# Kernel tuning notes

Measured on AMD Instinct MI355X. Metric: run time of the kernel, lower is better.

## Reference

```python
import jax, jax.numpy as jnp
import numpy as np

NHEAD = 16
EPS = 1e-5


def layer_norm(x, w, b):
    mu = jnp.mean(x, axis=-1, keepdims=True)
    var = jnp.var(x, axis=-1, keepdims=True)
    return (x - mu) * jax.lax.rsqrt(var + EPS) * w + b


def setup_inputs() -> dict:
    key = jax.random.key(0)
    ks = jax.random.split(key, 14)
    B, S, E, F = 16, 1024, 1024, 4096
    s = 0.02
    return {
        "x": jax.random.normal(ks[0], (B, S, E), jnp.float32),
        "in_proj_w": jax.random.normal(ks[1], (3 * E, E), jnp.float32) * s,
        "in_proj_b": jax.random.normal(ks[2], (3 * E,), jnp.float32) * s,
        "out_w": jax.random.normal(ks[3], (E, E), jnp.float32) * s,
        "out_b": jax.random.normal(ks[4], (E,), jnp.float32) * s,
        "lin1_w": jax.random.normal(ks[5], (F, E), jnp.float32) * s,
        "lin1_b": jax.random.normal(ks[6], (F,), jnp.float32) * s,
        "lin2_w": jax.random.normal(ks[7], (E, F), jnp.float32) * s,
        "lin2_b": jax.random.normal(ks[8], (E,), jnp.float32) * s,
        "norm1_w": jnp.ones((E,), jnp.float32),
        "norm1_b": jnp.zeros((E,), jnp.float32),
        "norm2_w": jnp.ones((E,), jnp.float32),
        "norm2_b": jnp.zeros((E,), jnp.float32),
    }


def reference(x, in_proj_w, in_proj_b, out_w, out_b, lin1_w, lin1_b, lin2_w, lin2_b,
              norm1_w, norm1_b, norm2_w, norm2_b):
    B, S, E = x.shape
    H = NHEAD
    D = E // H

    # --- pre-norm self-attention (q = k = v = norm1(x)) ---
    xn = layer_norm(x, norm1_w, norm1_b)
    qkv = xn @ in_proj_w.T + in_proj_b                      # [B,S,3E]
    q, k, v = jnp.split(qkv, 3, axis=-1)
    q = q.reshape(B, S, H, D)
    k = k.reshape(B, S, H, D)
    v = v.reshape(B, S, H, D)
    scale = 1.0 / jnp.sqrt(jnp.asarray(D, x.dtype))
    scores = jnp.einsum("bqhd,bkhd->bhqk", q, k) * scale    # [B,H,S,S]
    attn = jax.nn.softmax(scores, axis=-1)
    ctx = jnp.einsum("bhqk,bkhd->bqhd", attn, v).reshape(B, S, E)
    attn_out = ctx @ out_w.T + out_b
    x = x + attn_out

    # --- pre-norm feedforward (gelu) ---
    xn2 = layer_norm(x, norm2_w, norm2_b)
    h = jax.nn.gelu(xn2 @ lin1_w.T + lin1_b, approximate=False)
    x = x + (h @ lin2_w.T + lin2_b)
    return x
```

## Files before the change

### kernel.cpp

```cpp
#include <hip/hip_runtime.h>


typedef __attribute__((ext_vector_type(8))) short bf16x8;
typedef __attribute__((ext_vector_type(4))) float f32x4;
typedef __attribute__((ext_vector_type(8))) unsigned short u16x8;
typedef __attribute__((ext_vector_type(4))) unsigned short u16x4;

__device__ __forceinline__ float bf2f(unsigned short u) {
    return __uint_as_float(((unsigned int)u) << 16);
}
__device__ __forceinline__ unsigned short f2bf(float f) {
    unsigned int u = __float_as_uint(f);
    u += 0x7fffu + ((u >> 16) & 1u);
    return (unsigned short)(u >> 16);
}
__device__ __forceinline__ unsigned int pkbf_trunc(float a, float b) {
    return (__float_as_uint(a) >> 16) | (__float_as_uint(b) & 0xffff0000u);
}

__device__ __forceinline__ float fast_gelu(float v) {
    const float x = v * 0.70710678118654752f;
    const float ax = fabsf(x);
    const float t = __builtin_amdgcn_rcpf(fmaf(0.3275911f, ax, 1.0f));
    float p = fmaf(1.061405429f, t, -1.453152027f);
    p = fmaf(p, t, 1.421413741f);
    p = fmaf(p, t, -0.284496736f);
    p = fmaf(p, t, 0.254829592f);
    p = p * t;
    const float e = __expf(-x * x);
    float erfv = fmaf(-p, e, 1.0f);
    erfv = (x < 0.0f) ? -erfv : erfv;
    return 0.5f * v * (1.0f + erfv);
}

__device__ __forceinline__ void gload_lds16(const unsigned short* g, unsigned short* l) {
    __builtin_amdgcn_global_load_lds(
        (const __attribute__((address_space(1))) unsigned int*)g,
        (__attribute__((address_space(3))) unsigned int*)l, 16, 0, 0);
}

#define FENCE() asm volatile("" ::: "memory")
#define BAR()                         \
    do {                              \
        FENCE();                      \
        __builtin_amdgcn_s_barrier(); \
        FENCE();                      \
    } while (0)
#define VMCNT(n)                                               \
    do {                                                       \
        asm volatile("s_waitcnt vmcnt(" #n ")" ::: "memory");  \
        __builtin_amdgcn_sched_barrier(0);                     \
    } while (0)

__global__ __launch_bounds__(256) void cvt_kernel(const float* __restrict__ in,
                                                  unsigned short* __restrict__ out, int n4) {
    int i = blockIdx.x * 256 + threadIdx.x;
    if (i >= n4) return;
    float4 v = ((const float4*)in)[i];
    u16x4 o;
    o[0] = f2bf(v.x); o[1] = f2bf(v.y); o[2] = f2bf(v.z); o[3] = f2bf(v.w);
    ((u16x4*)out)[i] = o;
}

__global__ __launch_bounds__(256) void ln_kernel(const float* __restrict__ x,
                                                 const float* __restrict__ w,
                                                 const float* __restrict__ b,
                                                 unsigned short* __restrict__ out) {
    const int row = blockIdx.x;
    const int t = threadIdx.x;
    const float* xr = x + (size_t)row * 1024;
    float4 v = *(const float4*)(xr + t * 4);
    float s = v.x + v.y + v.z + v.w;
    float sq = v.x * v.x + v.y * v.y + v.z * v.z + v.w * v.w;
#pragma unroll
    for (int off = 32; off > 0; off >>= 1) {
        s += __shfl_xor(s, off);
        sq += __shfl_xor(sq, off);
    }
    __shared__ float rs_[4], rq_[4];
    if ((t & 63) == 0) { rs_[t >> 6] = s; rq_[t >> 6] = sq; }
    __syncthreads();
    s = rs_[0] + rs_[1] + rs_[2] + rs_[3];
    sq = rq_[0] + rq_[1] + rq_[2] + rq_[3];
    const float mu = s * (1.0f / 1024.0f);
    const float var = sq * (1.0f / 1024.0f) - mu * mu;
    const float rstd = rsqrtf(var + 1e-5f);
    const int c = t * 4;
    float4 wv = *(const float4*)(w + c);
    float4 bv = *(const float4*)(b + c);
    u16x4 o;
    o[0] = f2bf((v.x - mu) * rstd * wv.x + bv.x);
    o[1] = f2bf((v.y - mu) * rstd * wv.y + bv.y);
    o[2] = f2bf((v.z - mu) * rstd * wv.z + bv.z);
    o[3] = f2bf((v.w - mu) * rstd * wv.w + bv.w);
    *(u16x4*)(out + (size_t)row * 1024 + c) = o;
}

template <int EPI>
__global__ __launch_bounds__(512, 2) void gemm_bt(const unsigned short* __restrict__ A,
                                                  const unsigned short* __restrict__ Bt,
                                                  const float* __restrict__ bias,
                                                  const float* __restrict__ resid,
                                                  void* __restrict__ outp,
                                                  int M, int N, int K, int cnt,
                                                  int NC, int MC) {
    __shared__ __align__(16) unsigned short sA[2][256 * 64];
    __shared__ __align__(16) unsigned short sB[2][256 * 64];
    const int t = threadIdx.x;
    const int lane = t & 63;
    const int w = t >> 6;
    const int wm = w >> 2;
    const int wn = w & 3;
    const int quad = lane >> 4;
    const int cl = lane & 15;

    const int NB = gridDim.x;
    const int g = blockIdx.x;
    const int lpb = NB >> 3;
    const int xm = (g >> 2) & 1;
    const int xn = g & 3;
    const int l0 = g >> 3;

#define DECODE(tjv, mB, nB)                                  \
    do {                                                     \
        const int l_ = l0 + (tjv) * lpb;                     \
        const int mi_ = l_ / NC;                             \
        const int ni_ = l_ - mi_ * NC;                       \
        (mB) = (xm * MC + mi_) << 8;                         \
        (nB) = (xn * NC + ni_) << 8;                         \
    } while (0)

    const int swz0 = (quad ^ (cl & 7)) * 16;
    const int swz1 = ((quad + 4) ^ (cl & 7)) * 16;
    const char* aB0 = (const char*)sA + (wm * 128 + cl) * 128 + swz0;
    const char* aB1 = (const char*)sA + (wm * 128 + cl) * 128 + swz1;
    const char* bB0 = (const char*)sB + (wn * 64 + cl) * 128 + swz0;
    const char* bB1 = (const char*)sB + (wn * 64 + cl) * 128 + swz1;

    const int rl = lane >> 3;
    const size_t o8 = (size_t)8 * K;
    const size_t o128 = (size_t)128 * K;
    const size_t thr = (size_t)(w * 16 + rl) * K + (size_t)(((lane & 7) ^ rl) * 8);

#define STG(gp, sbuf, buf, hf, k0)                                                        \
    do {                                                                                  \
        gload_lds16((gp) + (k0) + thr + (hf) * o128,                                      \
                    &sbuf[buf][((hf) * 128 + w * 16) * 64]);                              \
        gload_lds16((gp) + (k0) + thr + (hf) * o128 + o8,                                 \
                    &sbuf[buf][((hf) * 128 + w * 16 + 8) * 64]);                          \
    } while (0)
#define READ_B8(buf)                                                                      \
    do {                                                                                  \
        _Pragma("unroll") for (int nf_ = 0; nf_ < 4; ++nf_) {                             \
            bfr[nf_][0] = *(const bf16x8*)(bB0 + (buf) * 32768 + nf_ * 2048);             \
            bfr[nf_][1] = *(const bf16x8*)(bB1 + (buf) * 32768 + nf_ * 2048);             \
        }                                                                                 \
    } while (0)
#define READ_A2(buf, mfb)                                                                 \
    do {                                                                                  \
        af[0][0] = *(const bf16x8*)(aB0 + (buf) * 32768 + (mfb) * 2048);                  \
        af[0][1] = *(const bf16x8*)(aB1 + (buf) * 32768 + (mfb) * 2048);                  \
        af[1][0] = *(const bf16x8*)(aB0 + (buf) * 32768 + ((mfb) + 1) * 2048);            \
        af[1][1] = *(const bf16x8*)(aB1 + (buf) * 32768 + ((mfb) + 1) * 2048);            \
    } while (0)
#define MFMA_Q(q)                                                                         \
    do {                                                                                  \
        __builtin_amdgcn_s_setprio(1);                                                    \
        _Pragma("unroll") for (int m_ = 0; m_ < 2; ++m_)                                  \
            _Pragma("unroll") for (int nf_ = 0; nf_ < 4; ++nf_)                           \
                _Pragma("unroll") for (int ks_ = 0; ks_ < 2; ++ks_)                       \
                    acc[2 * (q) + m_][nf_] = __builtin_amdgcn_mfma_f32_16x16x32_bf16(     \
                        bfr[nf_][ks_], af[m_][ks_], acc[2 * (q) + m_][nf_], 0, 0, 0);     \
        __builtin_amdgcn_s_setprio(0);                                                    \
    } while (0)

    f32x4 acc[8][4] = {};
    bf16x8 bfr[4][2];
    bf16x8 af[2][2];

    int mBc, nBc, mBn, nBn;
    DECODE(0, mBc, nBc);
    const unsigned short* gAc = A + (size_t)mBc * K;
    const unsigned short* gBc = Bt + (size_t)nBc * K;
    int kc = 0;
    mBn = mBc; nBn = nBc;
    const unsigned short* gAn = gAc;
    const unsigned short* gBn = gBc;
    int kn = 128;
    int tj = 0;

    STG(gAc, sA, 0, 0, kc); STG(gAc, sA, 0, 1, kc);
    STG(gBc, sB, 0, 0, kc); STG(gBc, sB, 0, 1, kc);
    STG(gBc, sB, 1, 0, kc + 64); STG(gBc, sB, 1, 1, kc + 64);
    VMCNT(4);
    BAR();

    const int TP = cnt * (K >> 7);
    for (int P = 0; P < TP; ++P) {
        const bool more = (P + 1 < TP);
        READ_B8(0); READ_A2(0, 0);
        STG(gAc, sA, 1, 0, kc + 64);
        BAR(); MFMA_Q(0);
        READ_A2(0, 2);
        STG(gAc, sA, 1, 1, kc + 64);
        BAR(); MFMA_Q(1);
        READ_A2(0, 4);
        if (more) STG(gBn, sB, 0, 0, kn);
        BAR(); MFMA_Q(2);
        READ_A2(0, 6);
        if (more) STG(gBn, sB, 0, 1, kn);
        BAR(); MFMA_Q(3);
        if (more) { VMCNT(4); } else { VMCNT(0); }
        BAR();
        READ_B8(1); READ_A2(1, 0);
        if (more) STG(gAn, sA, 0, 0, kn);
        BAR(); MFMA_Q(0);
        READ_A2(1, 2);
        if (more) STG(gAn, sA, 0, 1, kn);
        BAR(); MFMA_Q(1);
        READ_A2(1, 4);
        if (more) STG(gBn, sB, 1, 0, kn + 64);
        BAR(); MFMA_Q(2);
        READ_A2(1, 6);
        if (more) STG(gBn, sB, 1, 1, kn + 64);
        BAR(); MFMA_Q(3);
        if (more) VMCNT(4);
        BAR();

        if (kc + 128 == K) {
#pragma unroll
            for (int mf = 0; mf < 8; ++mf) {
                const int rowg = mBc + wm * 128 + mf * 16 + cl;
                const size_t rb = (size_t)rowg * N;
#pragma unroll
                for (int nf = 0; nf < 4; ++nf) {
                    const int colg = nBc + wn * 64 + nf * 16 + quad * 4;
                    const float4 bv = *(const float4*)(bias + colg);
                    const f32x4 a = acc[mf][nf];
                    const size_t idx = rb + colg;
                    if constexpr (EPI == 0) {
                        u16x4 o;
                        o[0] = f2bf(a[0] + bv.x); o[1] = f2bf(a[1] + bv.y);
                        o[2] = f2bf(a[2] + bv.z); o[3] = f2bf(a[3] + bv.w);
                        *(u16x4*)((unsigned short*)outp + idx) = o;
                    } else if constexpr (EPI == 1) {
                        const float4 rv = *(const float4*)(resid + idx);
                        float4 o;
                        o.x = a[0] + bv.x + rv.x; o.y = a[1] + bv.y + rv.y;
                        o.z = a[2] + bv.z + rv.z; o.w = a[3] + bv.w + rv.w;
                        *(float4*)((float*)outp + idx) = o;
                    } else {
                        u16x4 o;
                        o[0] = f2bf(fast_gelu(a[0] + bv.x));
                        o[1] = f2bf(fast_gelu(a[1] + bv.y));
                        o[2] = f2bf(fast_gelu(a[2] + bv.z));
                        o[3] = f2bf(fast_gelu(a[3] + bv.w));
                        *(u16x4*)((unsigned short*)outp + idx) = o;
                    }
                }
            }
            const f32x4 z = {0.f, 0.f, 0.f, 0.f};
#pragma unroll
            for (int mf = 0; mf < 8; ++mf)
#pragma unroll
                for (int nf = 0; nf < 4; ++nf) acc[mf][nf] = z;
        }
        kc = kn; gAc = gAn; gBc = gBn; mBc = mBn; nBc = nBn;
        kn += 128;
        if (kn >= K) {
            kn = 0;
            ++tj;
            if (tj < cnt) {
                DECODE(tj, mBn, nBn);
                gAn = A + (size_t)mBn * K;
                gBn = Bt + (size_t)nBn * K;
            }
        }
    }
#undef STG
#undef READ_B8
#undef READ_A2
#undef MFMA_Q
#undef DECODE
}

__global__ __launch_bounds__(256) void attn_mfma(const unsigned short* __restrict__ qkv,
                                                 unsigned short* __restrict__ ctx) {
    __shared__ __align__(16) unsigned short Ks[64 * 72];
    __shared__ __align__(16) unsigned int Vt[64 * 36];
    __shared__ __align__(16) unsigned short Ps[128 * 72];

    const int bh = blockIdx.x;
    const int qt = blockIdx.y;
    const int b = bh >> 4;
    const int h = bh & 15;
    const int t = threadIdx.x;
    const int w = t >> 6;
    const int lane = t & 63;
    const int quad = lane >> 4;
    const int cl = lane & 15;
    const size_t tok0 = (size_t)b * 1024;
    const int qrow0 = qt * 128 + w * 32;

    bf16x8 aq[2][2];
#pragma unroll
    for (int sub = 0; sub < 2; ++sub) {
        const unsigned short* qp =
            qkv + (tok0 + qrow0 + sub * 16 + cl) * 3072 + h * 64 + quad * 8;
        aq[sub][0] = *(const bf16x8*)(qp);
        aq[sub][1] = *(const bf16x8*)(qp + 32);
    }

    const bf16x8 vones = {0x3F80, 0x3F80, 0x3F80, 0x3F80, 0x3F80, 0x3F80, 0x3F80, 0x3F80};

    const int r0 = t >> 2;
    const int c16 = (t & 3) * 16;
    const int kp = t >> 3;
    const int dc = t & 7;

    f32x4 acc[2][5] = {};
    float m_r[2] = {-3.0e38f, -3.0e38f};

    for (int kt = 0; kt < 16; ++kt) {
        {
            const unsigned short* kg =
                qkv + (tok0 + kt * 64 + r0) * 3072 + 1024 + h * 64 + c16;
            *(int4*)(Ks + r0 * 72 + c16) = *(const int4*)(kg);
            *(int4*)(Ks + r0 * 72 + c16 + 8) = *(const int4*)(kg + 8);

            const unsigned short* vg =
                qkv + (tok0 + kt * 64 + 2 * kp) * 3072 + 2048 + h * 64 + dc * 8;
            u16x8 v0 = *(const u16x8*)(vg);
            u16x8 v1 = *(const u16x8*)(vg + 3072);
            const int g = kp >> 2, wd = kp & 3;
#pragma unroll
            for (int j = 0; j < 8; ++j) {
                const int d = dc * 8 + j;
                Vt[d * 36 + (((g ^ (d >> 3)) << 2) | wd)] =
                    ((unsigned int)v1[j] << 16) | (unsigned int)v0[j];
            }
        }
        __syncthreads();

#pragma unroll
        for (int sub = 0; sub < 2; ++sub) {
            f32x4 sc[4] = {};
#pragma unroll
            for (int i = 0; i < 4; ++i) {
                const int rb = i * 16 + cl;
#pragma unroll
                for (int ks = 0; ks < 2; ++ks) {
                    bf16x8 bk = *(const bf16x8*)(Ks + rb * 72 + quad * 8 + ks * 32);
                    sc[i] = __builtin_amdgcn_mfma_f32_16x16x32_bf16(bk, aq[sub][ks], sc[i],
                                                                    0, 0, 0);
                }
            }
            float mx0 = fmaxf(fmaxf(sc[0][0], sc[0][1]), fmaxf(sc[0][2], sc[0][3]));
            float mx1 = fmaxf(fmaxf(sc[1][0], sc[1][1]), fmaxf(sc[1][2], sc[1][3]));
            float mx2 = fmaxf(fmaxf(sc[2][0], sc[2][1]), fmaxf(sc[2][2], sc[2][3]));
            float mx3 = fmaxf(fmaxf(sc[3][0], sc[3][1]), fmaxf(sc[3][2], sc[3][3]));
            float rmax = fmaxf(fmaxf(mx0, mx1), fmaxf(mx2, mx3));
            rmax = fmaxf(rmax, __shfl_xor(rmax, 16));
            rmax = fmaxf(rmax, __shfl_xor(rmax, 32));
            const float mnew = fmaxf(m_r[sub], rmax * 0.125f);
            const float alpha = __expf(m_r[sub] - mnew);
            m_r[sub] = mnew;
            float al[4];
#pragma unroll
            for (int rr = 0; rr < 4; ++rr) al[rr] = __shfl(alpha, quad * 4 + rr, 16);
#pragma unroll
            for (int j = 0; j < 5; ++j)
#pragma unroll
                for (int rr = 0; rr < 4; ++rr) acc[sub][j][rr] *= al[rr];
            const unsigned short* pr = Ps + (w * 32 + sub * 16 + cl) * 72;
#pragma unroll
            for (int i = 0; i < 4; ++i) {
                const float p0 = __expf(fmaf(sc[i][0], 0.125f, -mnew));
                const float p1 = __expf(fmaf(sc[i][1], 0.125f, -mnew));
                const float p2 = __expf(fmaf(sc[i][2], 0.125f, -mnew));
                const float p3 = __expf(fmaf(sc[i][3], 0.125f, -mnew));
                uint2 pk;
                pk.x = pkbf_trunc(p0, p1);
                pk.y = pkbf_trunc(p2, p3);
                *(uint2*)(pr + i * 16 + quad * 4) = pk;
            }
        }

#pragma unroll
        for (int ks = 0; ks < 2; ++ks) {
            bf16x8 bv[4];
#pragma unroll
            for (int j = 0; j < 4; ++j) {
                const int d = j * 16 + cl;
                bv[j] = *(const bf16x8*)(Vt + d * 36 + (((quad + 4 * ks) ^ (d >> 3)) << 2));
            }
#pragma unroll
            for (int sub = 0; sub < 2; ++sub) {
                bf16x8 ap =
                    *(const bf16x8*)(Ps + (w * 32 + sub * 16 + cl) * 72 + quad * 8 + ks * 32);
#pragma unroll
                for (int j = 0; j < 4; ++j)
                    acc[sub][j] =
                        __builtin_amdgcn_mfma_f32_16x16x32_bf16(ap, bv[j], acc[sub][j], 0, 0, 0);
                acc[sub][4] =
                    __builtin_amdgcn_mfma_f32_16x16x32_bf16(ap, vones, acc[sub][4], 0, 0, 0);
            }
        }
        __syncthreads();
    }

#pragma unroll
    for (int sub = 0; sub < 2; ++sub)
#pragma unroll
        for (int rr = 0; rr < 4; ++rr) {
            const float inv = 1.0f / acc[sub][4][rr];
            const size_t tok = tok0 + qt * 128 + w * 32 + sub * 16 + quad * 4 + rr;
#pragma unroll
            for (int j = 0; j < 4; ++j)
                ctx[tok * 1024 + h * 64 + j * 16 + cl] = f2bf(acc[sub][j][rr] * inv);
        }
}

extern "C" void kernel_launch(void* const* d_in, const int* in_sizes, int n_in,
                              void* d_out, int out_size, void* d_ws, size_t ws_size,
                              hipStream_t stream) {
    const float* x    = (const float*)d_in[0];
    const float* wqkv = (const float*)d_in[1];
    const float* bqkv = (const float*)d_in[2];
    const float* wo   = (const float*)d_in[3];
    const float* bo   = (const float*)d_in[4];
    const float* w1   = (const float*)d_in[5];
    const float* b1   = (const float*)d_in[6];
    const float* w2   = (const float*)d_in[7];
    const float* b2   = (const float*)d_in[8];
    const float* n1w  = (const float*)d_in[9];
    const float* n1b  = (const float*)d_in[10];
    const float* n2w  = (const float*)d_in[11];
    const float* n2b  = (const float*)d_in[12];
    float* out = (float*)d_out;

    char* ws = (char*)d_ws;
    unsigned short* wqkv_b = (unsigned short*)(ws);
    unsigned short* wo_b   = (unsigned short*)(ws + 6291456);
    unsigned short* w1_b   = (unsigned short*)(ws + 8388608);
    unsigned short* w2_b   = (unsigned short*)(ws + 16777216);
    unsigned short* r1     = (unsigned short*)(ws + 25165824);
    unsigned short* r2     = (unsigned short*)(ws + 58720256);

    unsigned short* xn_b  = r1;
    unsigned short* ctx_b = r1;
    unsigned short* xn2_b = r1;
    unsigned short* qkv_b = r2;
    unsigned short* h_b   = r2;

    cvt_kernel<<<3072, 256, 0, stream>>>(wqkv, wqkv_b, 786432);
    cvt_kernel<<<1024, 256, 0, stream>>>(wo, wo_b, 262144);
    cvt_kernel<<<4096, 256, 0, stream>>>(w1, w1_b, 1048576);
    cvt_kernel<<<4096, 256, 0, stream>>>(w2, w2_b, 1048576);

    ln_kernel<<<16384, 256, 0, stream>>>(x, n1w, n1b, xn_b);
    gemm_bt<0><<<256, 512, 0, stream>>>(xn_b, wqkv_b, bqkv, nullptr, qkv_b,
                                        16384, 3072, 1024, 3, 3, 32);
    attn_mfma<<<dim3(256, 8), 256, 0, stream>>>(qkv_b, ctx_b);
    gemm_bt<1><<<256, 512, 0, stream>>>(ctx_b, wo_b, bo, x, out,
                                        16384, 1024, 1024, 1, 1, 32);
    ln_kernel<<<16384, 256, 0, stream>>>(out, n2w, n2b, xn2_b);

    if (ws_size >= 192937984ULL) {
        gemm_bt<2><<<256, 512, 0, stream>>>(xn2_b, w1_b, b1, nullptr, h_b,
                                            16384, 4096, 1024, 4, 4, 32);
        gemm_bt<1><<<256, 512, 0, stream>>>(h_b, w2_b, b2, out, out,
                                            16384, 1024, 4096, 1, 1, 32);
    } else {
        for (int c = 0; c < 2; ++c) {
            const size_t row0 = (size_t)c * 8192;
            gemm_bt<2><<<256, 512, 0, stream>>>(xn2_b + row0 * 1024, w1_b, b1,
                                                nullptr, h_b, 8192, 4096, 1024, 2, 4, 16);
            gemm_bt<1><<<128, 512, 0, stream>>>(h_b, w2_b, b2, out + row0 * 1024,
                                                out + row0 * 1024, 8192, 1024, 4096,
                                                1, 1, 16);
        }
    }
}
```

Before: 855.6 us.

## Enlarge attention tile to 256 queries, XOR-swizzle LDS, lazily rescale softmax

The attention kernel now runs 512 threads (8 waves) per block, each block covering 256 query rows, so every K/V tile staged in LDS is reused by twice as many queries and the grid is halved. K and P buffers drop their padding in favour of an XOR swizzle to avoid LDS bank conflicts, and K/V loading is redistributed across the larger thread count. The online-softmax rescale of the accumulators now runs only when the running max grows by more than a threshold, which skips most exp and multiply work. The lazy rescale lets probabilities exceed 1 by up to e^8 before normalisation, a small numerical risk with bf16 P values.

After: 789.8 us. -7.7%, faster.

```diff
diff --git a/kernel.cpp b/kernel.cpp
--- a/kernel.cpp
+++ b/kernel.cpp
@@ -284,11 +284,11 @@
 #undef DECODE
 }
 
-__global__ __launch_bounds__(256) void attn_mfma(const unsigned short* __restrict__ qkv,
+__global__ __launch_bounds__(512) void attn_mfma(const unsigned short* __restrict__ qkv,
                                                  unsigned short* __restrict__ ctx) {
-    __shared__ __align__(16) unsigned short Ks[64 * 72];
+    __shared__ __align__(16) unsigned short Ks[64 * 64];
     __shared__ __align__(16) unsigned int Vt[64 * 36];
-    __shared__ __align__(16) unsigned short Ps[128 * 72];
+    __shared__ __align__(16) unsigned short Ps[256 * 64];
 
     const int bh = blockIdx.x;
     const int qt = blockIdx.y;
@@ -299,8 +299,9 @@
     const int lane = t & 63;
     const int quad = lane >> 4;
     const int cl = lane & 15;
+    const int r7 = cl & 7;
     const size_t tok0 = (size_t)b * 1024;
-    const int qrow0 = qt * 128 + w * 32;
+    const int qrow0 = qt * 256 + w * 32;
 
     bf16x8 aq[2][2];
 #pragma unroll
@@ -313,10 +314,17 @@
 
     const bf16x8 vones = {0x3F80, 0x3F80, 0x3F80, 0x3F80, 0x3F80, 0x3F80, 0x3F80, 0x3F80};
 
-    const int r0 = t >> 2;
-    const int c16 = (t & 3) * 16;
-    const int kp = t >> 3;
-    const int dc = t & 7;
+    const int r0 = t >> 3;
+    const int c0 = t & 7;
+    const int kp = t >> 4;
+    const int dq = t & 15;
+
+    const char* kB0 = (const char*)Ks + cl * 128 + ((quad ^ r7) << 4);
+    const char* kB1 = (const char*)Ks + cl * 128 + (((quad + 4) ^ r7) << 4);
+    char* pb[2];
+#pragma unroll
+    for (int sub = 0; sub < 2; ++sub)
+        pb[sub] = (char*)Ps + (w * 32 + sub * 16 + cl) * 128;
 
     f32x4 acc[2][5] = {};
     float m_r[2] = {-3.0e38f, -3.0e38f};
@@ -324,19 +332,18 @@
     for (int kt = 0; kt < 16; ++kt) {
         {
             const unsigned short* kg =
-                qkv + (tok0 + kt * 64 + r0) * 3072 + 1024 + h * 64 + c16;
-            *(int4*)(Ks + r0 * 72 + c16) = *(const int4*)(kg);
-            *(int4*)(Ks + r0 * 72 + c16 + 8) = *(const int4*)(kg + 8);
+                qkv + (tok0 + kt * 64 + r0) * 3072 + 1024 + h * 64 + c0 * 8;
+            *(int4*)(Ks + r0 * 64 + ((c0 ^ (r0 & 7)) * 8)) = *(const int4*)(kg);
 
             const unsigned short* vg =
-                qkv + (tok0 + kt * 64 + 2 * kp) * 3072 + 2048 + h * 64 + dc * 8;
-            u16x8 v0 = *(const u16x8*)(vg);
-            u16x8 v1 = *(const u16x8*)(vg + 3072);
-            const int g = kp >> 2, wd = kp & 3;
-#pragma unroll
-            for (int j = 0; j < 8; ++j) {
-                const int d = dc * 8 + j;
-                Vt[d * 36 + (((g ^ (d >> 3)) << 2) | wd)] =
+                qkv + (tok0 + kt * 64 + 2 * kp) * 3072 + 2048 + h * 64 + dq * 4;
+            u16x4 v0 = *(const u16x4*)(vg);
+            u16x4 v1 = *(const u16x4*)(vg + 3072);
+            const int g2 = kp >> 2, wd = kp & 3;
+#pragma unroll
+            for (int j = 0; j < 4; ++j) {
+                const int d = dq * 4 + j;
+                Vt[d * 36 + (((g2 ^ (d >> 3)) << 2) | wd)] =
                     ((unsigned int)v1[j] << 16) | (unsigned int)v0[j];
             }
         }
@@ -347,13 +354,12 @@
             f32x4 sc[4] = {};
 #pragma unroll
             for (int i = 0; i < 4; ++i) {
-                const int rb = i * 16 + cl;
-#pragma unroll
-                for (int ks = 0; ks < 2; ++ks) {
-                    bf16x8 bk = *(const bf16x8*)(Ks + rb * 72 + quad * 8 + ks * 32);
-                    sc[i] = __builtin_amdgcn_mfma_f32_16x16x32_bf16(bk, aq[sub][ks], sc[i],
-                                                                    0, 0, 0);
-                }
+                bf16x8 bk0 = *(const bf16x8*)(kB0 + i * 2048);
+                bf16x8 bk1 = *(const bf16x8*)(kB1 + i * 2048);
+                sc[i] = __builtin_amdgcn_mfma_f32_16x16x32_bf16(bk0, aq[sub][0], sc[i],
+                                                                0, 0, 0);
+                sc[i] = __builtin_amdgcn_mfma_f32_16x16x32_bf16(bk1, aq[sub][1], sc[i],
+                                                                0, 0, 0);
             }
             float mx0 = fmaxf(fmaxf(sc[0][0], sc[0][1]), fmaxf(sc[0][2], sc[0][3]));
             float mx1 = fmaxf(fmaxf(sc[1][0], sc[1][1]), fmaxf(sc[1][2], sc[1][3]));
@@ -362,27 +368,31 @@
             float rmax = fmaxf(fmaxf(mx0, mx1), fmaxf(mx2, mx3));
             rmax = fmaxf(rmax, __shfl_xor(rmax, 16));
             rmax = fmaxf(rmax, __shfl_xor(rmax, 32));
-            const float mnew = fmaxf(m_r[sub], rmax * 0.125f);
-            const float alpha = __expf(m_r[sub] - mnew);
-            m_r[sub] = mnew;
-            float al[4];
-#pragma unroll
-            for (int rr = 0; rr < 4; ++rr) al[rr] = __shfl(alpha, quad * 4 + rr, 16);
-#pragma unroll
-            for (int j = 0; j < 5; ++j)
-#pragma unroll
-                for (int rr = 0; rr < 4; ++rr) acc[sub][j][rr] *= al[rr];
-            const unsigned short* pr = Ps + (w * 32 + sub * 16 + cl) * 72;
+            const float pm = rmax * 0.125f;
+            if (__any(pm > m_r[sub] + 8.0f)) {
+                const float mnew = fmaxf(m_r[sub], pm);
+                const float alpha = __expf(m_r[sub] - mnew);
+                m_r[sub] = mnew;
+                float al[4];
+#pragma unroll
+                for (int rr = 0; rr < 4; ++rr) al[rr] = __shfl(alpha, quad * 4 + rr, 16);
+#pragma unroll
+                for (int j = 0; j < 5; ++j)
+#pragma unroll
+                    for (int rr = 0; rr < 4; ++rr) acc[sub][j][rr] *= al[rr];
+            }
+            const float mcur = m_r[sub];
 #pragma unroll
             for (int i = 0; i < 4; ++i) {
-                const float p0 = __expf(fmaf(sc[i][0], 0.125f, -mnew));
-                const float p1 = __expf(fmaf(sc[i][1], 0.125f, -mnew));
-                const float p2 = __expf(fmaf(sc[i][2], 0.125f, -mnew));
-                const float p3 = __expf(fmaf(sc[i][3], 0.125f, -mnew));
+                const float p0 = __expf(fmaf(sc[i][0], 0.125f, -mcur));
+                const float p1 = __expf(fmaf(sc[i][1], 0.125f, -mcur));
+                const float p2 = __expf(fmaf(sc[i][2], 0.125f, -mcur));
+                const float p3 = __expf(fmaf(sc[i][3], 0.125f, -mcur));
                 uint2 pk;
                 pk.x = pkbf_trunc(p0, p1);
                 pk.y = pkbf_trunc(p2, p3);
-                *(uint2*)(pr + i * 16 + quad * 4) = pk;
+                *(uint2*)(pb[sub] + (((2 * i + (quad >> 1)) ^ r7) << 4) +
+                          ((quad & 1) << 3)) = pk;
             }
         }
 
@@ -396,8 +406,7 @@
             }
 #pragma unroll
             for (int sub = 0; sub < 2; ++sub) {
-                bf16x8 ap =
-                    *(const bf16x8*)(Ps + (w * 32 + sub * 16 + cl) * 72 + quad * 8 + ks * 32);
+                bf16x8 ap = *(const bf16x8*)(pb[sub] + (((quad + 4 * ks) ^ r7) << 4));
 #pragma unroll
                 for (int j = 0; j < 4; ++j)
                     acc[sub][j] =
@@ -414,7 +423,7 @@
 #pragma unroll
         for (int rr = 0; rr < 4; ++rr) {
             const float inv = 1.0f / acc[sub][4][rr];
-            const size_t tok = tok0 + qt * 128 + w * 32 + sub * 16 + quad * 4 + rr;
+            const size_t tok = tok0 + qrow0 + sub * 16 + quad * 4 + rr;
 #pragma unroll
             for (int j = 0; j < 4; ++j)
                 ctx[tok * 1024 + h * 64 + j * 16 + cl] = f2bf(acc[sub][j][rr] * inv);
@@ -461,7 +470,7 @@
     ln_kernel<<<16384, 256, 0, stream>>>(x, n1w, n1b, xn_b);
     gemm_bt<0><<<256, 512, 0, stream>>>(xn_b, wqkv_b, bqkv, nullptr, qkv_b,
                                         16384, 3072, 1024, 3, 3, 32);
-    attn_mfma<<<dim3(256, 8), 256, 0, stream>>>(qkv_b, ctx_b);
+    attn_mfma<<<dim3(256, 4), 512, 0, stream>>>(qkv_b, ctx_b);
     gemm_bt<1><<<256, 512, 0, stream>>>(ctx_b, wo_b, bo, x, out,
                                         16384, 1024, 1024, 1, 1, 32);
     ln_kernel<<<16384, 256, 0, stream>>>(out, n2w, n2b, xn2_b);
```
